# Performance work log

Hardware: AMD Instinct MI355X
Metric: run time of the kernel (lower is better)

## Reference

```python
import jax, jax.numpy as jnp
import numpy as np

B, S = 512, 1024          # batch sentences x tokens
VOCAB = 100000            # word alphabet size
CHAR_LEN = 32             # chars per word in lut
CHAR_VOCAB = 60           # char alphabet size
N_POS = 40                # POS tag set size
MAX_CANDS = 4000          # padded per-POS candidate list length
N_PRIV = 8                # first N_PRIV tags are privacy terms (e.g. NNP-like)
CTX_RATE = 0.15           # cfg.ctx_obf_rate
PRI_RATE = 1.0            # cfg.pri_obf_rate


def setup_inputs() -> dict:
    key = jax.random.key(0)
    ks = jax.random.split(key, 8)
    inp_word = jax.random.randint(ks[0], (B, S), 0, VOCAB, dtype=jnp.int32)
    inp_char = jax.random.randint(ks[1], (B, S, CHAR_LEN), 0, CHAR_VOCAB, dtype=jnp.int32)
    inp_pos = jax.random.randint(ks[2], (B, S), 0, N_POS, dtype=jnp.int32)
    inp_mask = jax.random.randint(ks[3], (B, S), 0, 2, dtype=jnp.int32)
    ctx_rand = jax.random.uniform(ks[4], (B, S), dtype=jnp.float32)
    pri_rand = jax.random.uniform(ks[5], (B, S), dtype=jnp.float32)
    cand_u = jax.random.uniform(ks[6], (B, S), dtype=jnp.float32)
    kl, kt, kc = jax.random.split(ks[7], 3)
    lut = jax.random.randint(kl, (VOCAB, CHAR_LEN), 0, CHAR_VOCAB, dtype=jnp.int32)
    tgt_table = jax.random.randint(kt, (N_POS, MAX_CANDS), 0, VOCAB, dtype=jnp.int32)
    counts = jax.random.randint(kc, (N_POS,), 1, MAX_CANDS, dtype=jnp.int32)
    priv_pos = jnp.arange(N_POS) < N_PRIV  # bool [N_POS]
    return {"inp_word": inp_word, "inp_char": inp_char, "inp_pos": inp_pos,
            "inp_mask": inp_mask, "ctx_rand": ctx_rand, "pri_rand": pri_rand,
            "cand_u": cand_u, "lut": lut, "tgt_table": tgt_table,
            "counts": counts, "priv_pos": priv_pos}


def reference(inp_word, inp_char, inp_pos, inp_mask, ctx_rand, pri_rand, cand_u,
              lut, tgt_table, counts, priv_pos):
    # pri_mask: union of pos_mask over privacy POS tags
    pri_mask = priv_pos[inp_pos]                      # bool [B,S]
    # Bernoulli obfuscation masks (torch.rand(shape) < rate)
    ctx_obf = ctx_rand < CTX_RATE                     # bool [B,S]
    pri_obf = pri_rand < PRI_RATE                     # bool [B,S]
    # per-token obf decision: privacy tags use pri_obf, context tags use ctx_obf
    obf_mask = jnp.where(pri_mask, pri_obf, ctx_obf)  # bool [B,S]
    # uniform random candidate from the token's POS candidate list
    cnt = counts[inp_pos]                             # int32 [B,S]
    idx = jnp.minimum((cand_u * cnt.astype(cand_u.dtype)).astype(jnp.int32),
                      cnt - 1)                        # [B,S] in [0, cnt)
    cdt = tgt_table[inp_pos, idx]                     # int32 [B,S]
    obf_word = jnp.where(obf_mask, cdt, inp_word)     # masked_scatter_ equivalent
    obf_char = lut[obf_word]                          # word_to_char gather [B,S,CHAR_LEN]
    cpy_mask = inp_mask.astype(bool) & (inp_word == obf_word)
    return (obf_word, inp_word, obf_char, inp_pos, obf_mask, pri_mask, cpy_mask)
```

## Files before the change

kernel.cpp:

```cpp
#include <hip/hip_runtime.h>

#define B_DIM 512
#define S_DIM 1024
#define NTOK (B_DIM * S_DIM)
#define CHAR_LEN 32
#define MAX_CANDS 4000
#define N_PRIV 8
#define CTX_RATE 0.15f


__global__ __launch_bounds__(256) void alltag_kernel(
    const int* __restrict__ inp_word,
    const int* __restrict__ inp_pos,
    const int* __restrict__ inp_mask,
    const float* __restrict__ ctx_rand,
    const float* __restrict__ pri_rand,
    const float* __restrict__ cand_u,
    const int4* __restrict__ lut4,
    const int* __restrict__ tgt_table,
    const int* __restrict__ counts,
    int* __restrict__ out)
{
    int t = blockIdx.x * blockDim.x + threadIdx.x;
    if (t >= NTOK * 8) return;
    int token = t >> 3;
    int sub   = t & 7;

    int pos  = inp_pos[token];
    int word = inp_word[token];
    bool pri_mask = (pos < N_PRIV);

    bool obf;
    if (pri_mask) obf = (pri_rand[token] < 1.0f);
    else          obf = (ctx_rand[token] < CTX_RATE);

    int obf_word = word;
    if (obf) {
        int cnt = counts[pos];
        int idx = (int)(cand_u[token] * (float)cnt);
        idx = min(idx, cnt - 1);
        obf_word = tgt_table[pos * MAX_CANDS + idx];
    }

    int4 v = lut4[obf_word * 8 + sub];
    int4* out_char4 = (int4*)(out + (size_t)NTOK * 2);
    out_char4[(size_t)token * 8 + sub] = v;

    if (sub == 0) {
        out[token]                      = obf_word;
        out[NTOK + token]               = word;
        out[(size_t)NTOK * 34 + token]  = pos;
        out[(size_t)NTOK * 35 + token]  = obf ? 1 : 0;
        out[(size_t)NTOK * 36 + token]  = pri_mask ? 1 : 0;
        bool cpy = (inp_mask[token] != 0) && (word == obf_word);
        out[(size_t)NTOK * 37 + token]  = cpy ? 1 : 0;
    }
}

extern "C" void kernel_launch(void* const* d_in, const int* in_sizes, int n_in,
                              void* d_out, int out_size, void* d_ws, size_t ws_size,
                              hipStream_t stream) {
    const int*   inp_word  = (const int*)  d_in[0];
    const int*   inp_pos   = (const int*)  d_in[2];
    const int*   inp_mask  = (const int*)  d_in[3];
    const float* ctx_rand  = (const float*)d_in[4];
    const float* pri_rand  = (const float*)d_in[5];
    const float* cand_u    = (const float*)d_in[6];
    const int4*  lut4      = (const int4*) d_in[7];
    const int*   tgt_table = (const int*)  d_in[8];
    const int*   counts    = (const int*)  d_in[9];
    int* out = (int*)d_out;

    const int total = NTOK * 8;
    const int block = 256;
    const int grid  = (total + block - 1) / block;
    alltag_kernel<<<grid, block, 0, stream>>>(inp_word, inp_pos, inp_mask,
                                              ctx_rand, pri_rand, cand_u,
                                              lut4, tgt_table, counts, out);
}
```

Baseline: 177.4 us.

## Process two tokens per thread with nontemporal loads/stores and branchless candidate lookup

Halves the grid so each thread handles two tokens spaced half the token range apart, giving more independent gathers in flight per thread. Streaming inputs and all outputs use nontemporal loads and stores so they bypass the cache and leave it to the LUT and candidate-table gathers. The candidate lookup now runs unconditionally and is selected afterwards, which removes divergence but adds table reads for tokens that are not obfuscated.

```diff
diff --git a/kernel.cpp b/kernel.cpp
--- a/kernel.cpp
+++ b/kernel.cpp
@@ -8,6 +8,52 @@
 #define N_PRIV 8
 #define CTX_RATE 0.15f
 
+typedef int vint4 __attribute__((ext_vector_type(4)));
+
+
+__device__ __forceinline__ void do_token(
+    int token, int sub,
+    const int* __restrict__ inp_word,
+    const int* __restrict__ inp_pos,
+    const int* __restrict__ inp_mask,
+    const float* __restrict__ ctx_rand,
+    const float* __restrict__ pri_rand,
+    const float* __restrict__ cand_u,
+    const vint4* __restrict__ lut4,
+    const int* __restrict__ tgt_table,
+    const int* __restrict__ counts,
+    int* __restrict__ out)
+{
+    int pos   = __builtin_nontemporal_load(&inp_pos[token]);
+    int word  = __builtin_nontemporal_load(&inp_word[token]);
+    float cr  = __builtin_nontemporal_load(&ctx_rand[token]);
+    float pr  = __builtin_nontemporal_load(&pri_rand[token]);
+    float cu  = __builtin_nontemporal_load(&cand_u[token]);
+
+    bool pri_mask = (pos < N_PRIV);
+    bool obf = pri_mask ? (pr < 1.0f) : (cr < CTX_RATE);
+
+    int cnt = counts[pos];
+    int idx = (int)(cu * (float)cnt);
+    idx = min(idx, cnt - 1);
+    int cdt = tgt_table[pos * MAX_CANDS + idx];
+    int obf_word = obf ? cdt : word;
+
+    vint4 v = lut4[obf_word * 8 + sub];
+    vint4* out_char4 = (vint4*)(out + (size_t)NTOK * 2);
+    __builtin_nontemporal_store(v, &out_char4[(size_t)token * 8 + sub]);
+
+    if (sub == 0) {
+        __builtin_nontemporal_store(obf_word, &out[token]);
+        __builtin_nontemporal_store(word, &out[NTOK + token]);
+        __builtin_nontemporal_store(pos, &out[(size_t)NTOK * 34 + token]);
+        __builtin_nontemporal_store(obf ? 1 : 0, &out[(size_t)NTOK * 35 + token]);
+        __builtin_nontemporal_store(pri_mask ? 1 : 0, &out[(size_t)NTOK * 36 + token]);
+        int msk = __builtin_nontemporal_load(&inp_mask[token]);
+        bool cpy = (msk != 0) && (word == obf_word);
+        __builtin_nontemporal_store(cpy ? 1 : 0, &out[(size_t)NTOK * 37 + token]);
+    }
+}
 
 __global__ __launch_bounds__(256) void alltag_kernel(
     const int* __restrict__ inp_word,
@@ -16,45 +62,20 @@
     const float* __restrict__ ctx_rand,
     const float* __restrict__ pri_rand,
     const float* __restrict__ cand_u,
-    const int4* __restrict__ lut4,
+    const vint4* __restrict__ lut4,
     const int* __restrict__ tgt_table,
     const int* __restrict__ counts,
     int* __restrict__ out)
 {
-    int t = blockIdx.x * blockDim.x + threadIdx.x;
-    if (t >= NTOK * 8) return;
-    int token = t >> 3;
-    int sub   = t & 7;
+    int g = blockIdx.x * blockDim.x + threadIdx.x;
+    int token0 = g >> 3;
+    int sub    = g & 7;
+    int token1 = token0 + (NTOK / 2);
 
-    int pos  = inp_pos[token];
-    int word = inp_word[token];
-    bool pri_mask = (pos < N_PRIV);
-
-    bool obf;
-    if (pri_mask) obf = (pri_rand[token] < 1.0f);
-    else          obf = (ctx_rand[token] < CTX_RATE);
-
-    int obf_word = word;
-    if (obf) {
-        int cnt = counts[pos];
-        int idx = (int)(cand_u[token] * (float)cnt);
-        idx = min(idx, cnt - 1);
-        obf_word = tgt_table[pos * MAX_CANDS + idx];
-    }
-
-    int4 v = lut4[obf_word * 8 + sub];
-    int4* out_char4 = (int4*)(out + (size_t)NTOK * 2);
-    out_char4[(size_t)token * 8 + sub] = v;
-
-    if (sub == 0) {
-        out[token]                      = obf_word;
-        out[NTOK + token]               = word;
-        out[(size_t)NTOK * 34 + token]  = pos;
-        out[(size_t)NTOK * 35 + token]  = obf ? 1 : 0;
-        out[(size_t)NTOK * 36 + token]  = pri_mask ? 1 : 0;
-        bool cpy = (inp_mask[token] != 0) && (word == obf_word);
-        out[(size_t)NTOK * 37 + token]  = cpy ? 1 : 0;
-    }
+    do_token(token0, sub, inp_word, inp_pos, inp_mask, ctx_rand, pri_rand,
+             cand_u, lut4, tgt_table, counts, out);
+    do_token(token1, sub, inp_word, inp_pos, inp_mask, ctx_rand, pri_rand,
+             cand_u, lut4, tgt_table, counts, out);
 }
 
 extern "C" void kernel_launch(void* const* d_in, const int* in_sizes, int n_in,
@@ -66,12 +87,12 @@
     const float* ctx_rand  = (const float*)d_in[4];
     const float* pri_rand  = (const float*)d_in[5];
     const float* cand_u    = (const float*)d_in[6];
-    const int4*  lut4      = (const int4*) d_in[7];
+    const vint4* lut4      = (const vint4*)d_in[7];
     const int*   tgt_table = (const int*)  d_in[8];
     const int*   counts    = (const int*)  d_in[9];
     int* out = (int*)d_out;
 
-    const int total = NTOK * 8;
+    const int total = NTOK * 4;
     const int block = 256;
     const int grid  = (total + block - 1) / block;
     alltag_kernel<<<grid, block, 0, stream>>>(inp_word, inp_pos, inp_mask,
```

Result: faster. 172.7 us (-2.6%).
